# Performance work log

Hardware: AMD Instinct MI355X
Metric: run time of the kernel (lower is better)

The kernel has to match this reference:

```python
import jax, jax.numpy as jnp
import numpy as np

N_NODES = 16000
N_EDGES = 512000
N_TYPES = 87      # atomic numbers covered by gfn2-xtb embedding
EMBED_DIM = 28    # 16s + 8p + 4d aux basis size
NODE_DIM = 128
NUM_BASIS = 20
CUTOFF = 5.0
P_ORDER = 5       # polynomial cutoff order
MUL0, MUL1, MUL2 = 128, 64, 32  # multiplicities of 0e, 1e, 2e irreps


def setup_inputs() -> dict:
    key = jax.random.key(0)
    k1, k2, k3, k4, k5, k6 = jax.random.split(key, 6)
    at_no = jax.random.randint(k1, (N_NODES,), 1, N_TYPES)
    # spread atoms so edge distances cover (0, cutoff] and beyond
    pos = jax.random.normal(k2, (N_NODES, 3), dtype=jnp.float32) * 3.0
    src = jax.random.randint(k3, (N_EDGES,), 0, N_NODES)
    off = jax.random.randint(k4, (N_EDGES,), 1, N_NODES)  # guarantee src != dst (no zero dist)
    dst = (src + off) % N_NODES
    edge_index = jnp.stack([src, dst])
    embed_table = jax.random.normal(k5, (N_TYPES, EMBED_DIM), dtype=jnp.float32)
    W = jax.random.normal(k6, (NODE_DIM, EMBED_DIM), dtype=jnp.float32) / np.float32(np.sqrt(EMBED_DIM))
    b = jnp.zeros((NODE_DIM,), dtype=jnp.float32)  # nn.init.zeros_(bias)
    return {"at_no": at_no, "pos": pos, "edge_index": edge_index,
            "embed_table": embed_table, "W": W, "b": b}


def _sph_harm_lmax2(u):
    """e3nn real spherical harmonics l=0,1,2, normalize=True (u is unit), 'component' norm."""
    x, y, z = u[..., 0], u[..., 1], u[..., 2]
    sh0 = jnp.ones_like(x)[..., None]                       # [E,1]
    s3 = np.float32(np.sqrt(3.0))
    sh1 = s3 * u                                            # [E,3]
    s15 = np.float32(np.sqrt(15.0))
    s5 = np.float32(np.sqrt(5.0))
    sh2 = jnp.stack([
        s15 * x * z,
        s15 * x * y,
        s5 * (y * y - 0.5 * (x * x + z * z)),
        s15 * y * z,
        0.5 * s15 * (z * z - x * x),
    ], axis=-1)                                             # [E,5]
    return sh0, sh1, sh2


def reference(at_no, pos, edge_index, embed_table, W, b):
    pos = pos[:, jnp.array([1, 2, 0])]                      # axis permutation from forward()
    vec = pos[edge_index[0]] - pos[edge_index[1]]           # [E,3] edge gather
    dist = jnp.linalg.norm(vec, axis=-1, keepdims=True)     # [E,1]

    # scalar node features: Int2c1e embedding lookup + Linear
    x_scalar = embed_table[at_no] @ W.T + b                 # [N,128]

    # Bessel RBF: sqrt(2/c) * sin(n*pi*d/c) / d, n = 1..num_basis
    n = jnp.arange(1, NUM_BASIS + 1, dtype=pos.dtype)
    rbf = np.float32(np.sqrt(2.0 / CUTOFF)) * jnp.sin(n * jnp.pi * dist / CUTOFF) / dist  # [E,20]

    # polynomial cutoff (DimeNet-style, order p)
    u = dist / CUTOFF
    p = float(P_ORDER)
    ca = -(p + 1.0) * (p + 2.0) / 2.0
    cb = p * (p + 2.0)
    cc = -p * (p + 1.0) / 2.0
    fcut = jnp.where(u < 1.0,
                     1.0 + ca * u ** P_ORDER + cb * u ** (P_ORDER + 1) + cc * u ** (P_ORDER + 2),
                     0.0)                                   # [E,1]

    # real spherical harmonics on unit edge vectors, tiled per irrep multiplicity
    unit = vec / dist
    sh0, sh1, sh2 = _sph_harm_lmax2(unit)
    rsh = jnp.concatenate([jnp.tile(sh0, (1, MUL0)),
                           jnp.tile(sh1, (1, MUL1)),
                           jnp.tile(sh2, (1, MUL2))], axis=-1)  # [E, 480]

    return x_scalar, rbf, fcut, rsh
```

## Files before the change

### kernel.cpp

```cpp
#include <hip/hip_runtime.h>
#include <math.h>

#define N_NODES   16000
#define N_EDGES   512000
#define EMBED_DIM 28
#define NODE_DIM  128
#define NUM_BASIS 20

#define EPB  256
#define NBLK (N_EDGES / EPB)

typedef float f32x4 __attribute__((ext_vector_type(4)));

__global__ __launch_bounds__(256) void node_kernel(
    const int*   __restrict__ at_no,
    const float* __restrict__ embed,
    const float* __restrict__ W,
    const float* __restrict__ b,
    float*       __restrict__ out)
{
    int idx = blockIdx.x * 256 + threadIdx.x;
    if (idx >= N_NODES * NODE_DIM) return;
    int node = idx >> 7;
    int d    = idx & 127;
    int a    = at_no[node];
    const float* er = embed + a * EMBED_DIM;
    const float* wr = W + d * EMBED_DIM;
    float sum = b[d];
#pragma unroll
    for (int k = 0; k < EMBED_DIM; ++k)
        sum = fmaf(er[k], wr[k], sum);
    out[idx] = sum;
}

__global__ __launch_bounds__(256) void fused_edge_kernel(
    const float* __restrict__ pos,
    const int*   __restrict__ eidx,
    float*       __restrict__ rbf,
    float*       __restrict__ fcut,
    float*       __restrict__ rsh)
{
    __shared__ float    sh_shv[EPB * 12];
    __shared__ float    sh_rbf[EPB * 20];
    __shared__ unsigned sh_sel[120];

    const int t  = threadIdx.x;
    const int e0 = blockIdx.x * EPB;
    const int e  = e0 + t;

    if (t < 120) {
        unsigned pack = 0;
#pragma unroll
        for (int k = 0; k < 4; ++k) {
            int col = 4 * t + k;
            int jj;
            if (col < 128)      jj = 0;
            else if (col < 320) jj = 1 + (col - 128) % 3;
            else                jj = 4 + (col - 320) % 5;
            pack |= (unsigned)(jj * 4) << (8 * k);
        }
        sh_sel[t] = pack;
    }

    {
        int s  = eidx[e];
        int dn = eidx[N_EDGES + e];

        float ax = pos[s*3+1],  ay = pos[s*3+2],  az = pos[s*3+0];
        float bx = pos[dn*3+1], by = pos[dn*3+2], bz = pos[dn*3+0];
        float vx = ax - bx, vy = ay - by, vz = az - bz;
        float dist = sqrtf(vx*vx + vy*vy + vz*vz);
        float inv  = 1.0f / dist;
        float ux = vx*inv, uy = vy*inv, uz = vz*inv;

        const float S3  = 1.7320508075688772f;
        const float S5  = 2.2360679774997896f;
        const float S15 = 3.8729833462074170f;

        float* r = sh_shv + t * 12;
        r[0] = 1.0f;
        r[1] = S3 * ux;  r[2] = S3 * uy;  r[3] = S3 * uz;
        r[4] = S15 * ux * uz;
        r[5] = S15 * ux * uy;
        r[6] = S5  * (uy*uy - 0.5f*(ux*ux + uz*uz));
        r[7] = S15 * uy * uz;
        r[8] = 0.5f * S15 * (uz*uz - ux*ux);

        float u  = dist * 0.2f;
        float u2 = u*u, u5 = u2*u2*u;
        float f  = 1.0f + u5*(-21.0f + u*(35.0f - 15.0f*u));
        fcut[e] = (u < 1.0f) ? f : 0.0f;

        float th = 0.62831853071795864769f * dist;
        float s1 = __sinf(th), c1 = __cosf(th);
        float twoc = 2.0f * c1;
        float kk = 0.6324555320336759f * inv;
        float sp = 0.0f, sc = s1;
        float* rb = sh_rbf + t * 20;
#pragma unroll
        for (int q = 0; q < NUM_BASIS; ++q) {
            rb[q] = kk * sc;
            float nx = twoc*sc - sp; sp = sc; sc = nx;
        }
    }
    __syncthreads();

    {
        const f32x4* ls = (const f32x4*)sh_rbf;
        f32x4* go = (f32x4*)(rbf + (size_t)e0 * NUM_BASIS);
#pragma unroll
        for (int q = 0; q < 5; ++q)
            go[q * EPB + t] = ls[q * EPB + t];
    }

    {
        int le = t / 120;
        int c  = t - le * 120;
        float* outp = rsh + (size_t)e0 * 480 + (size_t)t * 4;

#pragma unroll 2
        for (int i = 0; i < 120; ++i) {
            unsigned pk = sh_sel[c];
            const char* row = (const char*)(sh_shv + le * 12);
            f32x4 v;
            v.x = *(const float*)(row + (pk & 0xffu));
            v.y = *(const float*)(row + ((pk >> 8) & 0xffu));
            v.z = *(const float*)(row + ((pk >> 16) & 0xffu));
            v.w = *(const float*)(row + (pk >> 24));
            *(f32x4*)outp = v;
            outp += 256 * 4;
            c += 16; le += 2;
            if (c >= 120) { c -= 120; le += 1; }
        }
    }
}

extern "C" void kernel_launch(void* const* d_in, const int* in_sizes, int n_in,
                              void* d_out, int out_size, void* d_ws, size_t ws_size,
                              hipStream_t stream) {
    const int*   at_no = (const int*)  d_in[0];
    const float* pos   = (const float*)d_in[1];
    const int*   eidx  = (const int*)  d_in[2];
    const float* embed = (const float*)d_in[3];
    const float* W     = (const float*)d_in[4];
    const float* b     = (const float*)d_in[5];

    float* out      = (float*)d_out;
    float* x_scalar = out;
    float* rbf      = x_scalar + (size_t)N_NODES * NODE_DIM;
    float* fcut     = rbf + (size_t)N_EDGES * NUM_BASIS;
    float* rsh      = fcut + N_EDGES;

    node_kernel<<<(N_NODES * NODE_DIM + 255) / 256, 256, 0, stream>>>(
        at_no, embed, W, b, x_scalar);

    fused_edge_kernel<<<NBLK, 256, 0, stream>>>(
        pos, eidx, rbf, fcut, rsh);
}
```

Measured before the change: 216.4 us.

## Precompute rotated SH patterns in LDS so rsh store reads single float4

Each edge thread now writes nine pre-rotated float4 patterns of its spherical-harmonic values into shared memory. The rsh output loop then does one aligned float4 LDS read per store, using per-thread offsets computed once, in place of four scalar gathers through a packed selector table. The block size drops to 128 edges, and rbf values are written to LDS as float4s. The aim is to cut LDS instruction count and index arithmetic in the store loop. The cost is more shared memory per edge and a 15-entry offset array held in registers.

```diff
diff --git a/kernel.cpp b/kernel.cpp
--- a/kernel.cpp
+++ b/kernel.cpp
@@ -7,8 +7,11 @@
 #define NODE_DIM  128
 #define NUM_BASIS 20
 
-#define EPB  256
-#define NBLK (N_EDGES / EPB)
+#define EPB   128
+#define NBLK  (N_EDGES / EPB)
+
+#define PSTRIDE 516
+#define PAT_DWORDS (8 * PSTRIDE + EPB * 4)
 
 typedef float f32x4 __attribute__((ext_vector_type(4)));
 
@@ -33,34 +36,19 @@
     out[idx] = sum;
 }
 
-__global__ __launch_bounds__(256) void fused_edge_kernel(
+__global__ __launch_bounds__(128) void fused_edge_kernel(
     const float* __restrict__ pos,
     const int*   __restrict__ eidx,
     float*       __restrict__ rbf,
     float*       __restrict__ fcut,
     float*       __restrict__ rsh)
 {
-    __shared__ float    sh_shv[EPB * 12];
-    __shared__ float    sh_rbf[EPB * 20];
-    __shared__ unsigned sh_sel[120];
+    __shared__ float sh_pat[PAT_DWORDS];
+    __shared__ float sh_rbf[EPB * 20];
 
     const int t  = threadIdx.x;
     const int e0 = blockIdx.x * EPB;
     const int e  = e0 + t;
-
-    if (t < 120) {
-        unsigned pack = 0;
-#pragma unroll
-        for (int k = 0; k < 4; ++k) {
-            int col = 4 * t + k;
-            int jj;
-            if (col < 128)      jj = 0;
-            else if (col < 320) jj = 1 + (col - 128) % 3;
-            else                jj = 4 + (col - 320) % 5;
-            pack |= (unsigned)(jj * 4) << (8 * k);
-        }
-        sh_sel[t] = pack;
-    }
 
     {
         int s  = eidx[e];
@@ -76,15 +64,26 @@
         const float S3  = 1.7320508075688772f;
         const float S5  = 2.2360679774997896f;
         const float S15 = 3.8729833462074170f;
+        float s0 = S3 * ux, s1 = S3 * uy, s2 = S3 * uz;
+        float t0 = S15 * ux * uz;
+        float t1 = S15 * ux * uy;
+        float t2 = S5  * (uy*uy - 0.5f*(ux*ux + uz*uz));
+        float t3 = S15 * uy * uz;
+        float t4 = 0.5f * S15 * (uz*uz - ux*ux);
 
-        float* r = sh_shv + t * 12;
-        r[0] = 1.0f;
-        r[1] = S3 * ux;  r[2] = S3 * uy;  r[3] = S3 * uz;
-        r[4] = S15 * ux * uz;
-        r[5] = S15 * ux * uy;
-        r[6] = S5  * (uy*uy - 0.5f*(ux*ux + uz*uz));
-        r[7] = S15 * uy * uz;
-        r[8] = 0.5f * S15 * (uz*uz - ux*ux);
+        f32x4* pb = (f32x4*)(sh_pat) + t;
+#define PW(j, a_, b_, c_, d_) { f32x4 v_; v_.x=a_; v_.y=b_; v_.z=c_; v_.w=d_; \
+                                pb[(j) * (PSTRIDE/4)] = v_; }
+        PW(0, 1.0f, 1.0f, 1.0f, 1.0f)
+        PW(1, s0, s1, s2, s0)
+        PW(2, s1, s2, s0, s1)
+        PW(3, s2, s0, s1, s2)
+        PW(4, t0, t1, t2, t3)
+        PW(5, t1, t2, t3, t4)
+        PW(6, t2, t3, t4, t0)
+        PW(7, t3, t4, t0, t1)
+        PW(8, t4, t0, t1, t2)
+#undef PW
 
         float u  = dist * 0.2f;
         float u2 = u*u, u5 = u2*u2*u;
@@ -92,15 +91,19 @@
         fcut[e] = (u < 1.0f) ? f : 0.0f;
 
         float th = 0.62831853071795864769f * dist;
-        float s1 = __sinf(th), c1 = __cosf(th);
-        float twoc = 2.0f * c1;
+        float sn = __sinf(th), cs = __cosf(th);
+        float twoc = 2.0f * cs;
         float kk = 0.6324555320336759f * inv;
-        float sp = 0.0f, sc = s1;
-        float* rb = sh_rbf + t * 20;
+        float sp = 0.0f, sc = sn;
+        f32x4* rb = (f32x4*)(sh_rbf + t * 20);
 #pragma unroll
-        for (int q = 0; q < NUM_BASIS; ++q) {
-            rb[q] = kk * sc;
-            float nx = twoc*sc - sp; sp = sc; sc = nx;
+        for (int q = 0; q < 5; ++q) {
+            f32x4 v_;
+            v_.x = kk * sc; { float nx = twoc*sc - sp; sp = sc; sc = nx; }
+            v_.y = kk * sc; { float nx = twoc*sc - sp; sp = sc; sc = nx; }
+            v_.z = kk * sc; { float nx = twoc*sc - sp; sp = sc; sc = nx; }
+            v_.w = kk * sc; { float nx = twoc*sc - sp; sp = sc; sc = nx; }
+            rb[q] = v_;
         }
     }
     __syncthreads();
@@ -114,23 +117,31 @@
     }
 
     {
-        int le = t / 120;
-        int c  = t - le * 120;
-        float* outp = rsh + (size_t)e0 * 480 + (size_t)t * 4;
+        int offs[15];
+#pragma unroll
+        for (int k = 0; k < 15; ++k) {
+            int u  = k * 128 + t;
+            int d  = u / 120;
+            int c  = u - d * 120;
+            int p;
+            if (c < 32)      p = 0;
+            else if (c < 80) p = 1 + (c - 32) % 3;
+            else             p = 4 + (4 * (c - 80)) % 5;
+            offs[k] = p * PSTRIDE + d * 4;
+        }
 
-#pragma unroll 2
-        for (int i = 0; i < 120; ++i) {
-            unsigned pk = sh_sel[c];
-            const char* row = (const char*)(sh_shv + le * 12);
-            f32x4 v;
-            v.x = *(const float*)(row + (pk & 0xffu));
-            v.y = *(const float*)(row + ((pk >> 8) & 0xffu));
-            v.z = *(const float*)(row + ((pk >> 16) & 0xffu));
-            v.w = *(const float*)(row + (pk >> 24));
-            *(f32x4*)outp = v;
-            outp += 256 * 4;
-            c += 16; le += 2;
-            if (c >= 120) { c -= 120; le += 1; }
+        float* outb = rsh + (size_t)e0 * 480 + (size_t)t * 4;
+        int base = 0;
+
+#pragma unroll 1
+        for (int i = 0; i < 8; ++i) {
+#pragma unroll
+            for (int k = 0; k < 15; ++k) {
+                f32x4 v = *(const f32x4*)(sh_pat + base + offs[k]);
+                *(f32x4*)(outb + (size_t)k * 512) = v;
+            }
+            base += 64;
+            outb += 15 * 512;
         }
     }
 }
@@ -154,6 +165,6 @@
     node_kernel<<<(N_NODES * NODE_DIM + 255) / 256, 256, 0, stream>>>(
         at_no, embed, W, b, x_scalar);
 
-    fused_edge_kernel<<<NBLK, 256, 0, stream>>>(
+    fused_edge_kernel<<<NBLK, 128, 0, stream>>>(
         pos, eidx, rbf, fcut, rsh);
 }
```

New measurement: 217.2 us. No clear change (+0.3%).
